# Kernel tuning notes

Measured on AMD Instinct MI355X. Metric: run time of the kernel, lower is better.

Reference implementation:

```python
import jax, jax.numpy as jnp
import numpy as np

N = 100000   # nodes
E = 1600000  # edges
IN = 64      # in_channels
H = 64       # hidden_channels
OUT = 2      # out_channels
EPS = 1e-5   # BatchNorm eps


def setup_inputs() -> dict:
    key = jax.random.key(0)
    ks = jax.random.split(key, 14)
    x = jax.random.normal(ks[0], (N, IN), dtype=jnp.float32)
    edge_index = jax.random.randint(ks[1], (2, E), 0, N, dtype=jnp.int64)

    def lin(k, shape, fan_in):
        return (jax.random.normal(k, shape, dtype=jnp.float32) / np.float32(np.sqrt(fan_in)))

    return {
        "x": x,
        "edge_index": edge_index,
        "W0": lin(ks[2], (IN, H), IN),
        "b0": jnp.zeros((H,), jnp.float32),
        "g0": jnp.ones((H,), jnp.float32),
        "be0": jnp.zeros((H,), jnp.float32),
        "W1": lin(ks[3], (H, H), H),
        "b1": jnp.zeros((H,), jnp.float32),
        "g1": jnp.ones((H,), jnp.float32),
        "be1": jnp.zeros((H,), jnp.float32),
        "W2": lin(ks[4], (H, OUT), H),
        "b2": jnp.zeros((OUT,), jnp.float32),
    }


def _gcn_conv(h_in, W, b, src, dst, norm):
    # GCNConv: linear transform, then D^-1/2 (A + I) D^-1/2 aggregation, then bias
    h = h_in @ W                                   # [N, d_out]
    msg = h[src] * norm[:, None]                   # gather + scale, [E+N, d_out]
    agg = jax.ops.segment_sum(msg, dst, num_segments=N)
    return agg + b


def _batch_norm(h, gamma, beta):
    # training-mode BatchNorm1d over the node dimension (biased variance)
    mean = jnp.mean(h, axis=0)
    var = jnp.mean(jnp.square(h - mean), axis=0)
    return (h - mean) * jax.lax.rsqrt(var + EPS) * gamma + beta


def reference(x, edge_index, W0, b0, g0, be0, W1, b1, g1, be1, W2, b2):
    loop = jnp.arange(N, dtype=edge_index.dtype)
    src = jnp.concatenate([edge_index[0], loop])   # self loops appended
    dst = jnp.concatenate([edge_index[1], loop])
    deg = jax.ops.segment_sum(jnp.ones_like(dst, dtype=jnp.float32), dst, num_segments=N)
    dinv = jax.lax.rsqrt(deg)                      # deg >= 1 due to self loops
    norm = dinv[src] * dinv[dst]                   # [E+N]

    h = jax.nn.relu(_batch_norm(_gcn_conv(x, W0, b0, src, dst, norm), g0, be0))
    h_res = h
    h = jax.nn.relu(_batch_norm(_gcn_conv(h, W1, b1, src, dst, norm), g1, be1))
    h = h + h_res                                  # residual add
    out = _gcn_conv(h, W2, b2, src, dst, norm)     # [N, OUT]
    return out
```

## Files before the change

kernel.cpp:

```cpp
#include <hip/hip_runtime.h>


#define NN 100000
#define NE 1600000
#define NBUCK 1563
#define NBLK 256
#define CHUNK 6250
#define MAXB 2048

typedef unsigned short ushort_t;

__device__ __forceinline__ ushort_t f2bf(float f) {
    unsigned u = __float_as_uint(f);
    unsigned r = u + 0x7FFFu + ((u >> 16) & 1u);
    return (ushort_t)(r >> 16);
}
__device__ __forceinline__ float bflo(unsigned u) { return __uint_as_float(u << 16); }
__device__ __forceinline__ float bfhi(unsigned u) { return __uint_as_float(u & 0xFFFF0000u); }

__launch_bounds__(1024)
__global__ void kA_hist(const int* __restrict__ dst, int* __restrict__ H) {
    __shared__ int h[NBUCK];
    int t = threadIdx.x, blk = blockIdx.x;
    for (int b = t; b < NBUCK; b += 1024) h[b] = 0;
    __syncthreads();
    int e0 = blk * CHUNK;
    for (int e = e0 + t; e < e0 + CHUNK; e += 1024) atomicAdd(&h[dst[e] >> 6], 1);
    __syncthreads();
    for (int b = t; b < NBUCK; b += 1024) H[b * NBLK + blk] = h[b];
}
__launch_bounds__(256)
__global__ void kB1(const int* __restrict__ H, int* __restrict__ bsum) {
    __shared__ int sh[256];
    int b = blockIdx.x, t = threadIdx.x;
    sh[t] = H[b * NBLK + t];
    __syncthreads();
    for (int s = 128; s; s >>= 1) {
        if (t < s) sh[t] += sh[t + s];
        __syncthreads();
    }
    if (t == 0) bsum[b] = sh[0];
}
__global__ void kB2(const int* __restrict__ bsum, int* __restrict__ bbase) {
    __shared__ int part[256];
    int t = threadIdx.x;
    int loc[7];
    int s = 0;
#pragma unroll
    for (int k = 0; k < 7; ++k) {
        int i = t * 7 + k;
        int v = (i < NBUCK) ? bsum[i] : 0;
        loc[k] = s;
        s += v;
    }
    part[t] = s;
    __syncthreads();
    if (t == 0) {
        int acc = 0;
        for (int i = 0; i < 256; ++i) { int v = part[i]; part[i] = acc; acc += v; }
        bbase[NBUCK] = acc;
    }
    __syncthreads();
    int base = part[t];
#pragma unroll
    for (int k = 0; k < 7; ++k) {
        int i = t * 7 + k;
        if (i < NBUCK) bbase[i] = base + loc[k];
    }
}
__launch_bounds__(256)
__global__ void kB3(int* __restrict__ H, const int* __restrict__ bbase) {
    __shared__ int sh[256];
    int b = blockIdx.x, t = threadIdx.x;
    sh[t] = H[b * NBLK + t];
    __syncthreads();
    if (t == 0) {
        int acc = bbase[b];
        for (int i = 0; i < 256; ++i) { int v = sh[i]; sh[i] = acc; acc += v; }
    }
    __syncthreads();
    H[b * NBLK + t] = sh[t];
}
__launch_bounds__(256)
__global__ void kC_scatter(const int* __restrict__ src, const int* __restrict__ dst,
                           const int* __restrict__ O, unsigned int* __restrict__ sp) {
    __shared__ int cur[NBUCK];
    int t = threadIdx.x, blk = blockIdx.x;
    for (int b = t; b < NBUCK; b += 256) cur[b] = O[b * NBLK + blk];
    __syncthreads();
    int e0 = blk * CHUNK;
    for (int e = e0 + t; e < e0 + CHUNK; e += 256) {
        int d = dst[e], s = src[e];
        int p = atomicAdd(&cur[d >> 6], 1);
        sp[p] = ((unsigned int)(d & 63) << 24) | (unsigned int)s;
    }
}
__launch_bounds__(256)
__global__ void kD2_fin(const unsigned int* __restrict__ sp, const int* __restrict__ bbase,
                        int* __restrict__ csrc, int* __restrict__ rowstart,
                        int* __restrict__ cntg, float* __restrict__ dinv) {
    __shared__ int cnt[64], ofs[64], cur[64];
    __shared__ int tmp[MAXB];
    int b = blockIdx.x, t = threadIdx.x;
    int beg = bbase[b], end = bbase[b + 1], n = end - beg;
    if (t < 64) cnt[t] = 0;
    __syncthreads();
    for (int i = beg + t; i < end; i += 256) atomicAdd(&cnt[sp[i] >> 24], 1);
    __syncthreads();
    if (t == 0) {
        int acc = 0;
        for (int k = 0; k < 64; ++k) { int v = cnt[k]; ofs[k] = acc; cur[k] = acc; acc += v; }
    }
    __syncthreads();
    int node = b * 64 + t;
    if (t < 64 && node < NN) {
        rowstart[node] = beg + ofs[t];
        cntg[node] = cnt[t];
        dinv[node] = rsqrtf((float)(cnt[t] + 1));
    }
    if (n <= MAXB) {
        for (int i = beg + t; i < end; i += 256) {
            unsigned int v = sp[i];
            int p = atomicAdd(&cur[v >> 24], 1);
            tmp[p] = (int)(v & 0xFFFFFFu);
        }
        __syncthreads();
        for (int i = t; i < n; i += 256) csrc[beg + i] = tmp[i];
    } else {
        for (int i = beg + t; i < end; i += 256) {
            unsigned int v = sp[i];
            int p = atomicAdd(&cur[v >> 24], 1);
            csrc[beg + p] = (int)(v & 0xFFFFFFu);
        }
    }
}

template <int MODE>
__launch_bounds__(256, 4)
__global__ void k_gemm64(const float* __restrict__ X, const float* __restrict__ W,
                         const float* __restrict__ stats, const float* __restrict__ g,
                         const float* __restrict__ be, const float* __restrict__ dinv,
                         ushort_t* __restrict__ Yb, float* __restrict__ side) {
    __shared__ float xs[4][68];
    int t = threadIdx.x;
    int c = t & 63, rr = t >> 6;
    float w[64];
#pragma unroll
    for (int k = 0; k < 64; ++k) w[k] = W[k * 64 + c];
    float scale = 1.f, shift = 0.f;
    if (MODE == 1) {
        float mean = stats[c] * (1.0f / NN);
        float var = stats[64 + c] * (1.0f / NN) - mean * mean;
        scale = g[c] * rsqrtf(var + 1e-5f);
        shift = be[c] - mean * scale;
    }
    int base = blockIdx.x * 64;
#pragma unroll 2
    for (int rb = 0; rb < 16; ++rb) {
        int row = base + rb * 4 + rr;
        if (row >= NN) continue;
        float v = X[row * 64 + c];
        if (MODE == 1) {
            v = fmaxf(fmaf(v, scale, shift), 0.f);
            side[row * 64 + c] = v;
        }
        xs[rr][c] = v;
        const float4* xp = (const float4*)xs[rr];
        float a0 = 0.f, a1 = 0.f, a2 = 0.f, a3 = 0.f;
#pragma unroll
        for (int k4 = 0; k4 < 16; ++k4) {
            float4 xv = xp[k4];
            a0 = fmaf(xv.x, w[k4 * 4 + 0], a0);
            a1 = fmaf(xv.y, w[k4 * 4 + 1], a1);
            a2 = fmaf(xv.z, w[k4 * 4 + 2], a2);
            a3 = fmaf(xv.w, w[k4 * 4 + 3], a3);
        }
        Yb[row * 64 + c] = f2bf(dinv[row] * ((a0 + a1) + (a2 + a3)));
    }
}

#define ACC8(q)                                                   \
    acc0.x += bflo(q.x); acc0.y += bfhi(q.x);                     \
    acc0.z += bflo(q.y); acc0.w += bfhi(q.y);                     \
    acc1.x += bflo(q.z); acc1.y += bfhi(q.z);                     \
    acc1.z += bflo(q.w); acc1.w += bfhi(q.w);

__launch_bounds__(256)
__global__ void k_agg_csr(const ushort_t* __restrict__ Yb, const int* __restrict__ rowstart,
                          const int* __restrict__ cnt, const int* __restrict__ csrc,
                          const float* __restrict__ dinv, float* __restrict__ agg) {
    int wid = (blockIdx.x * blockDim.x + threadIdx.x) >> 6;
    int lane = threadIdx.x & 63;
    if (wid >= NN) return;
    int grp = lane >> 3;
    int l8 = lane & 7;
    int beg = rowstart[wid], n = cnt[wid];
    float4 acc0 = {0.f, 0.f, 0.f, 0.f}, acc1 = {0.f, 0.f, 0.f, 0.f};
    if (grp == 0) {
        uint4 q = ((const uint4*)(Yb + (long)wid * 64))[l8];
        ACC8(q);
    }
    int j = grp;
    for (; j + 8 < n; j += 16) {
        int s0 = csrc[beg + j];
        int s1 = csrc[beg + j + 8];
        uint4 q0 = ((const uint4*)(Yb + (long)s0 * 64))[l8];
        uint4 q1 = ((const uint4*)(Yb + (long)s1 * 64))[l8];
        ACC8(q0);
        ACC8(q1);
    }
    if (j < n) {
        int s = csrc[beg + j];
        uint4 q = ((const uint4*)(Yb + (long)s * 64))[l8];
        ACC8(q);
    }
#pragma unroll
    for (int m = 8; m <= 32; m <<= 1) {
        acc0.x += __shfl_xor(acc0.x, m);
        acc0.y += __shfl_xor(acc0.y, m);
        acc0.z += __shfl_xor(acc0.z, m);
        acc0.w += __shfl_xor(acc0.w, m);
        acc1.x += __shfl_xor(acc1.x, m);
        acc1.y += __shfl_xor(acc1.y, m);
        acc1.z += __shfl_xor(acc1.z, m);
        acc1.w += __shfl_xor(acc1.w, m);
    }
    if (grp == 0) {
        float d = dinv[wid];
        float4 r0 = {acc0.x * d, acc0.y * d, acc0.z * d, acc0.w * d};
        float4 r1 = {acc1.x * d, acc1.y * d, acc1.z * d, acc1.w * d};
        ((float4*)(agg + (long)wid * 64))[l8 * 2] = r0;
        ((float4*)(agg + (long)wid * 64))[l8 * 2 + 1] = r1;
    }
}

__launch_bounds__(256)
__global__ void k_bn_stats(const float* __restrict__ X, float* __restrict__ stats) {
    __shared__ float sh[512];
    int t = threadIdx.x;
    int c = t & 63, rr = t >> 6;
    float sum = 0.f, sq = 0.f;
    for (int r = blockIdx.x * 4 + rr; r < NN; r += gridDim.x * 4) {
        float v = X[r * 64 + c];
        sum += v;
        sq = fmaf(v, v, sq);
    }
    sh[t] = sum;
    sh[256 + t] = sq;
    __syncthreads();
    if (t < 64) {
        float s = sh[t] + sh[t + 64] + sh[t + 128] + sh[t + 192];
        float q = sh[256 + t] + sh[320 + t] + sh[384 + t] + sh[448 + t];
        atomicAdd(&stats[t], s);
        atomicAdd(&stats[64 + t], q);
    }
}

__launch_bounds__(256)
__global__ void k_gemm_out2(const float* __restrict__ X, const float* __restrict__ stats,
                            const float* __restrict__ g, const float* __restrict__ be,
                            const float* __restrict__ R, const float* __restrict__ W2,
                            const float* __restrict__ dinv, float* __restrict__ Tp) {
    int t = threadIdx.x;
    int lane = t & 63, wv = t >> 6;
    int row = blockIdx.x * 4 + wv;
    if (row >= NN) return;
    float mean = stats[lane] * (1.0f / NN);
    float var = stats[64 + lane] * (1.0f / NN) - mean * mean;
    float scale = g[lane] * rsqrtf(var + 1e-5f);
    float shift = be[lane] - mean * scale;
    float w0 = W2[lane * 2], w1 = W2[lane * 2 + 1];
    float v = X[row * 64 + lane];
    v = fmaxf(fmaf(v, scale, shift), 0.f) + R[row * 64 + lane];
    float p0 = v * w0, p1 = v * w1;
#pragma unroll
    for (int s = 32; s; s >>= 1) {
        p0 += __shfl_xor(p0, s);
        p1 += __shfl_xor(p1, s);
    }
    if (lane == 0) {
        float d = dinv[row];
        Tp[row * 2] = d * p0;
        Tp[row * 2 + 1] = d * p1;
    }
}

__launch_bounds__(256)
__global__ void k_out_csr(const float* __restrict__ Tp, const int* __restrict__ rowstart,
                          const int* __restrict__ cnt, const int* __restrict__ csrc,
                          const float* __restrict__ dinv, const float* __restrict__ b2,
                          float* __restrict__ out) {
    int id = blockIdx.x * blockDim.x + threadIdx.x;
    int node = id >> 3, l = id & 7;
    if (node >= NN) return;
    int beg = rowstart[node], n = cnt[node];
    float a0 = 0.f, a1 = 0.f;
    if (l == 0) { a0 = Tp[node * 2]; a1 = Tp[node * 2 + 1]; }
    for (int j = l; j < n; j += 8) {
        int s = csrc[beg + j];
        a0 += Tp[s * 2];
        a1 += Tp[s * 2 + 1];
    }
#pragma unroll
    for (int m = 1; m < 8; m <<= 1) {
        a0 += __shfl_xor(a0, m);
        a1 += __shfl_xor(a1, m);
    }
    if (l == 0) {
        float d = dinv[node];
        out[node * 2] = d * a0 + b2[0];
        out[node * 2 + 1] = d * a1 + b2[1];
    }
}

extern "C" void kernel_launch(void* const* d_in, const int* in_sizes, int n_in,
                              void* d_out, int out_size, void* d_ws, size_t ws_size,
                              hipStream_t stream) {
    const float* x   = (const float*)d_in[0];
    const int*   ei  = (const int*)d_in[1];
    const int*   src = ei;
    const int*   dst = ei + NE;
    const float* W0  = (const float*)d_in[2];
    const float* g0  = (const float*)d_in[4];
    const float* be0 = (const float*)d_in[5];
    const float* W1  = (const float*)d_in[6];
    const float* g1  = (const float*)d_in[8];
    const float* be1 = (const float*)d_in[9];
    const float* W2  = (const float*)d_in[10];
    const float* b2  = (const float*)d_in[11];
    float* out = (float*)d_out;

    int*   H      = (int*)d_ws;
    int*   bsum   = H + NBUCK * NBLK;
    int*   bbase  = bsum + 2048;
    unsigned int* sp = (unsigned int*)(bbase + 2048);
    int*   csrc   = (int*)(sp + NE);
    int*   rowstart = csrc + NE;
    int*   cntg   = rowstart + NN;
    float* dinv   = (float*)(cntg + NN);
    ushort_t* Ab  = (ushort_t*)(dinv + NN);
    float* B      = (float*)(Ab + NN * 64);
    float* C      = B + NN * 64;
    float* Tp     = C + NN * 64;
    float* stats0 = Tp + NN * 2;
    float* stats1 = stats0 + 128;

    hipMemsetAsync(stats0, 0, 256 * sizeof(float), stream);

    kA_hist<<<NBLK, 1024, 0, stream>>>(dst, H);
    kB1<<<NBUCK, 256, 0, stream>>>(H, bsum);
    kB2<<<1, 256, 0, stream>>>(bsum, bbase);
    kB3<<<NBUCK, 256, 0, stream>>>(H, bbase);
    kC_scatter<<<NBLK, 256, 0, stream>>>(src, dst, H, sp);
    kD2_fin<<<NBUCK, 256, 0, stream>>>(sp, bbase, csrc, rowstart, cntg, dinv);

    int gemmGrid = (NN + 63) / 64;
    int aggGrid  = (NN * 64) / 256;

    k_gemm64<0><<<gemmGrid, 256, 0, stream>>>(x, W0, nullptr, nullptr, nullptr, dinv, Ab, nullptr);
    k_agg_csr<<<aggGrid, 256, 0, stream>>>(Ab, rowstart, cntg, csrc, dinv, B);
    k_bn_stats<<<1024, 256, 0, stream>>>(B, stats0);

    k_gemm64<1><<<gemmGrid, 256, 0, stream>>>(B, W1, stats0, g0, be0, dinv, Ab, C);
    k_agg_csr<<<aggGrid, 256, 0, stream>>>(Ab, rowstart, cntg, csrc, dinv, B);
    k_bn_stats<<<1024, 256, 0, stream>>>(B, stats1);

    k_gemm_out2<<<(NN + 3) / 4, 256, 0, stream>>>(B, stats1, g1, be1, C, W2, dinv, Tp);
    k_out_csr<<<(NN * 8 + 255) / 256, 256, 0, stream>>>(Tp, rowstart, cntg, csrc, dinv, b2, out);
}
```

Before: 376.4 us.

## Replace scalar FP32 node GEMMs with bf16 MFMA 16x16x32 tiles

Rewrites the two 64x64 feature-transform kernels to use bf16 MFMA instructions. Each wave handles two 16-row tiles, with W held in registers as bf16 fragments and X loaded as vectorized float4s and converted to bf16. The BN+ReLU prologue and the side store are vectorized. This targets the per-row scalar FMA loops and their LDS staging, but rounds the GEMM inputs to bf16, which costs some accuracy.

```diff
diff --git a/kernel.cpp b/kernel.cpp
--- a/kernel.cpp
+++ b/kernel.cpp
@@ -9,6 +9,8 @@
 #define MAXB 2048
 
 typedef unsigned short ushort_t;
+typedef __attribute__((ext_vector_type(8))) short bf16x8;
+typedef __attribute__((ext_vector_type(4))) float f32x4;
 
 __device__ __forceinline__ ushort_t f2bf(float f) {
     unsigned u = __float_as_uint(f);
@@ -137,45 +139,96 @@
 
 template <int MODE>
 __launch_bounds__(256, 4)
-__global__ void k_gemm64(const float* __restrict__ X, const float* __restrict__ W,
-                         const float* __restrict__ stats, const float* __restrict__ g,
-                         const float* __restrict__ be, const float* __restrict__ dinv,
-                         ushort_t* __restrict__ Yb, float* __restrict__ side) {
-    __shared__ float xs[4][68];
+__global__ void k_gemm_mfma(const float* __restrict__ X, const float* __restrict__ W,
+                            const float* __restrict__ stats, const float* __restrict__ g,
+                            const float* __restrict__ be, const float* __restrict__ dinv,
+                            ushort_t* __restrict__ Yb, float* __restrict__ side) {
     int t = threadIdx.x;
-    int c = t & 63, rr = t >> 6;
-    float w[64];
-#pragma unroll
-    for (int k = 0; k < 64; ++k) w[k] = W[k * 64 + c];
-    float scale = 1.f, shift = 0.f;
+    int lane = t & 63, wv = t >> 6;
+    int m = lane & 15;
+    int kg = lane >> 4;
+
+    bf16x8 bfr[4][2];
+#pragma unroll
+    for (int ct = 0; ct < 4; ++ct)
+#pragma unroll
+        for (int kf = 0; kf < 2; ++kf)
+#pragma unroll
+            for (int e = 0; e < 8; ++e) {
+                int k = kf * 32 + kg * 8 + e;
+                bfr[ct][kf][e] = (short)f2bf(W[k * 64 + ct * 16 + m]);
+            }
+
+    float sc[2][8], sh[2][8];
     if (MODE == 1) {
-        float mean = stats[c] * (1.0f / NN);
-        float var = stats[64 + c] * (1.0f / NN) - mean * mean;
-        scale = g[c] * rsqrtf(var + 1e-5f);
-        shift = be[c] - mean * scale;
-    }
-    int base = blockIdx.x * 64;
-#pragma unroll 2
-    for (int rb = 0; rb < 16; ++rb) {
-        int row = base + rb * 4 + rr;
-        if (row >= NN) continue;
-        float v = X[row * 64 + c];
-        if (MODE == 1) {
-            v = fmaxf(fmaf(v, scale, shift), 0.f);
-            side[row * 64 + c] = v;
+#pragma unroll
+        for (int kf = 0; kf < 2; ++kf) {
+            int k0 = kf * 32 + kg * 8;
+            const f32x4* s4 = (const f32x4*)(stats + k0);
+            const f32x4* q4 = (const f32x4*)(stats + 64 + k0);
+            const f32x4* g4 = (const f32x4*)(g + k0);
+            const f32x4* b4 = (const f32x4*)(be + k0);
+#pragma unroll
+            for (int h = 0; h < 2; ++h) {
+                f32x4 sv = s4[h], qv = q4[h], gv = g4[h], bv = b4[h];
+#pragma unroll
+                for (int e2 = 0; e2 < 4; ++e2) {
+                    float mean = sv[e2] * (1.0f / NN);
+                    float var = qv[e2] * (1.0f / NN) - mean * mean;
+                    float s = gv[e2] * rsqrtf(var + 1e-5f);
+                    sc[kf][h * 4 + e2] = s;
+                    sh[kf][h * 4 + e2] = bv[e2] - mean * s;
+                }
+            }
         }
-        xs[rr][c] = v;
-        const float4* xp = (const float4*)xs[rr];
-        float a0 = 0.f, a1 = 0.f, a2 = 0.f, a3 = 0.f;
-#pragma unroll
-        for (int k4 = 0; k4 < 16; ++k4) {
-            float4 xv = xp[k4];
-            a0 = fmaf(xv.x, w[k4 * 4 + 0], a0);
-            a1 = fmaf(xv.y, w[k4 * 4 + 1], a1);
-            a2 = fmaf(xv.z, w[k4 * 4 + 2], a2);
-            a3 = fmaf(xv.w, w[k4 * 4 + 3], a3);
+    }
+
+    int tile0 = blockIdx.x * 8 + wv * 2;
+#pragma unroll
+    for (int tt = 0; tt < 2; ++tt) {
+        int row0 = (tile0 + tt) * 16;
+        if (row0 >= NN) break;
+        long arow = row0 + m;
+        bf16x8 afr[2];
+#pragma unroll
+        for (int kf = 0; kf < 2; ++kf) {
+            const f32x4* xp = (const f32x4*)(X + arow * 64 + kf * 32 + kg * 8);
+            f32x4 v0 = xp[0], v1 = xp[1];
+            if (MODE == 1) {
+#pragma unroll
+                for (int e = 0; e < 4; ++e) {
+                    v0[e] = fmaxf(fmaf(v0[e], sc[kf][e], sh[kf][e]), 0.f);
+                    v1[e] = fmaxf(fmaf(v1[e], sc[kf][e + 4], sh[kf][e + 4]), 0.f);
+                }
+                f32x4* sp2 = (f32x4*)(side + arow * 64 + kf * 32 + kg * 8);
+                sp2[0] = v0;
+                sp2[1] = v1;
+            }
+#pragma unroll
+            for (int e = 0; e < 4; ++e) {
+                afr[kf][e] = (short)f2bf(v0[e]);
+                afr[kf][e + 4] = (short)f2bf(v1[e]);
+            }
         }
-        Yb[row * 64 + c] = f2bf(dinv[row] * ((a0 + a1) + (a2 + a3)));
+        f32x4 acc0 = {0.f, 0.f, 0.f, 0.f}, acc1 = acc0, acc2 = acc0, acc3 = acc0;
+        acc0 = __builtin_amdgcn_mfma_f32_16x16x32_bf16(afr[0], bfr[0][0], acc0, 0, 0, 0);
+        acc0 = __builtin_amdgcn_mfma_f32_16x16x32_bf16(afr[1], bfr[0][1], acc0, 0, 0, 0);
+        acc1 = __builtin_amdgcn_mfma_f32_16x16x32_bf16(afr[0], bfr[1][0], acc1, 0, 0, 0);
+        acc1 = __builtin_amdgcn_mfma_f32_16x16x32_bf16(afr[1], bfr[1][1], acc1, 0, 0, 0);
+        acc2 = __builtin_amdgcn_mfma_f32_16x16x32_bf16(afr[0], bfr[2][0], acc2, 0, 0, 0);
+        acc2 = __builtin_amdgcn_mfma_f32_16x16x32_bf16(afr[1], bfr[2][1], acc2, 0, 0, 0);
+        acc3 = __builtin_amdgcn_mfma_f32_16x16x32_bf16(afr[0], bfr[3][0], acc3, 0, 0, 0);
+        acc3 = __builtin_amdgcn_mfma_f32_16x16x32_bf16(afr[1], bfr[3][1], acc3, 0, 0, 0);
+#pragma unroll
+        for (int r = 0; r < 4; ++r) {
+            int grow = row0 + kg * 4 + r;
+            float dd = dinv[grow];
+            long gb = (long)grow * 64 + m;
+            Yb[gb] = f2bf(dd * acc0[r]);
+            Yb[gb + 16] = f2bf(dd * acc1[r]);
+            Yb[gb + 32] = f2bf(dd * acc2[r]);
+            Yb[gb + 48] = f2bf(dd * acc3[r]);
+        }
     }
 }
 
@@ -354,14 +407,14 @@
     kC_scatter<<<NBLK, 256, 0, stream>>>(src, dst, H, sp);
     kD2_fin<<<NBUCK, 256, 0, stream>>>(sp, bbase, csrc, rowstart, cntg, dinv);
 
-    int gemmGrid = (NN + 63) / 64;
+    int mfmaGrid = 782;
     int aggGrid  = (NN * 64) / 256;
 
-    k_gemm64<0><<<gemmGrid, 256, 0, stream>>>(x, W0, nullptr, nullptr, nullptr, dinv, Ab, nullptr);
+    k_gemm_mfma<0><<<mfmaGrid, 256, 0, stream>>>(x, W0, nullptr, nullptr, nullptr, dinv, Ab, nullptr);
     k_agg_csr<<<aggGrid, 256, 0, stream>>>(Ab, rowstart, cntg, csrc, dinv, B);
     k_bn_stats<<<1024, 256, 0, stream>>>(B, stats0);
 
-    k_gemm64<1><<<gemmGrid, 256, 0, stream>>>(B, W1, stats0, g0, be0, dinv, Ab, C);
+    k_gemm_mfma<1><<<mfmaGrid, 256, 0, stream>>>(B, W1, stats0, g0, be0, dinv, Ab, C);
     k_agg_csr<<<aggGrid, 256, 0, stream>>>(Ab, rowstart, cntg, csrc, dinv, B);
     k_bn_stats<<<1024, 256, 0, stream>>>(B, stats1);
 
```

Result: faster. 344.6 us (-8.4%).
